# Performance work log

Measured on AMD Instinct MI355X. Metric: run time of the kernel, lower is better.

## Reference

```python
import jax, jax.numpy as jnp
import numpy as np

B, T, F, H = 256, 128, 256, 512

def _unif(key, shape, fan_in):
    stv = 1.0 / np.sqrt(fan_in)
    return jax.random.uniform(key, shape, jnp.float32, -stv, stv)

def setup_inputs() -> dict:
    key = jax.random.key(0)
    ks = jax.random.split(key, 20)
    x = jax.random.normal(ks[0], (B, T, F), jnp.float32)
    mask = (jax.random.uniform(ks[1], (B, T, F)) < 0.8).astype(jnp.float32)
    deltas = jax.random.uniform(ks[2], (B, T, F), jnp.float32) * 5.0
    return {
        'x': x, 'mask': mask, 'deltas': deltas,
        'W_gh': _unif(ks[3], (H, F), F), 'b_gh': jnp.zeros((H,), jnp.float32),
        'w_gx': _unif(ks[4], (F,), F), 'b_gx': jnp.zeros((F,), jnp.float32),
        'W_hist': _unif(ks[5], (F, H), H), 'b_hist': jnp.zeros((F,), jnp.float32),
        'W_fr': _unif(ks[6], (F, F), F), 'b_fr': jnp.zeros((F,), jnp.float32),
        'W_comb': _unif(ks[7], (F, 2 * F), 2 * F), 'b_comb': jnp.zeros((F,), jnp.float32),
        'W_ih': _unif(ks[8], (4 * H, 2 * F), 2 * F), 'b_ih': jnp.zeros((4 * H,), jnp.float32),
        'W_hh': _unif(ks[9], (4 * H, H), H), 'b_hh': jnp.zeros((4 * H,), jnp.float32),
    }

def reference(x, mask, deltas, W_gh, b_gh, w_gx, b_gx, W_hist, b_hist,
              W_fr, b_fr, W_comb, b_comb, W_ih, b_ih, W_hh, b_hh):
    dtype = x.dtype
    Fdim = x.shape[2]
    W_fr_m = W_fr * (1.0 - jnp.eye(Fdim, dtype=dtype))

    def step(carry, inp):
        h, c, loss = carry
        x_t, m_t, d_t = inp  # each [B, F]
        gamma_h = jnp.exp(-jax.nn.relu(d_t @ W_gh.T + b_gh))       # [B, H]
        h = h * gamma_h
        x_h = h @ W_hist.T + b_hist                                 # [B, F]
        x_r = m_t * x_t + (1.0 - m_t) * x_h
        xu = x_r @ W_fr_m.T + b_fr                                  # [B, F]
        gamma_x = jnp.exp(-jax.nn.relu(d_t * w_gx + b_gx))          # diag Decay
        beta = jax.nn.sigmoid(jnp.concatenate([gamma_x, m_t], axis=1) @ W_comb.T + b_comb)
        x_comb = beta * xu + (1.0 - beta) * x_h
        # MAE on observed entries, per step, accumulated
        loss = loss + jnp.sum(jnp.abs(x_comb - x_t) * m_t) / (jnp.sum(m_t) + 1e-12)
        x_imp = m_t * x_t + (1.0 - m_t) * x_comb
        rnn_in = jnp.concatenate([x_imp, m_t], axis=1)              # [B, 2F]
        gates = rnn_in @ W_ih.T + b_ih + h @ W_hh.T + b_hh          # [B, 4H]
        i_g, f_g, g_g, o_g = jnp.split(gates, 4, axis=1)
        i_g = jax.nn.sigmoid(i_g); f_g = jax.nn.sigmoid(f_g)
        g_g = jnp.tanh(g_g);       o_g = jax.nn.sigmoid(o_g)
        c = f_g * c + i_g * g_g
        h = o_g * jnp.tanh(c)
        return (h, c, loss), (x_imp, x_comb)

    Bdim, Hdim = x.shape[0], W_hh.shape[1]
    init = (jnp.zeros((Bdim, Hdim), dtype), jnp.zeros((Bdim, Hdim), dtype), jnp.zeros((), dtype))
    xs = (x.transpose(1, 0, 2), mask.transpose(1, 0, 2), deltas.transpose(1, 0, 2))
    (h, c, x_loss), (x_imp_seq, rec_seq) = jax.lax.scan(step, init, xs)
    x_imp = x_imp_seq.transpose(1, 0, 2)          # [B, T, F]
    reconstruction = rec_seq.transpose(1, 0, 2)   # [B, T, F]
    kl = jnp.zeros((), dtype)                     # non-bayesian
    return x_imp, reconstruction, h, x_loss, kl
```

## Files before the change

kernel.cpp:

```cpp
#include <hip/hip_runtime.h>
#include <hip/hip_bf16.h>

typedef float f32x4 __attribute__((ext_vector_type(4)));
typedef __bf16 bf16x8 __attribute__((ext_vector_type(8)));
typedef short s16x8 __attribute__((ext_vector_type(8)));
typedef unsigned short u16;
typedef unsigned long long u64;
typedef unsigned char u8;

constexpr int Bb = 256, Tt = 128, Ff = 256, Hh = 512;
constexpr int TF = Tt * Ff;
constexpr long OFF_RECON = (long)Bb * Tt * Ff;
constexpr long OFF_H     = 2L * Bb * Tt * Ff;
constexpr long OFF_LOSS  = OFF_H + (long)Bb * Hh;

__device__ inline float sigf(float v){ return 1.f / (1.f + expf(-v)); }
__device__ inline u16 f2b(float f){
  unsigned u = __float_as_uint(f);
  u += 0x7fffu + ((u >> 16) & 1u);
  return (u16)(u >> 16);
}
__device__ inline float b2f(u16 b){ return __uint_as_float(((unsigned)b) << 16); }

__device__ inline unsigned f2e4_sw(float f){
  unsigned u = __float_as_uint(f);
  unsigned s = (u >> 24) & 0x80u;
  int e = (int)((u >> 23) & 0xff) - 127;
  unsigned m = u & 0x7fffffu;
  if (((u >> 23) & 0xff) == 0xff) return s | 0x7e;
  if (e > 8 || (e == 8 && m > 0x600000)) return s | 0x7e;
  if (e < -10) return s;
  if (e >= -6) {
    unsigned keep = m >> 20, rest = m & 0xfffffu;
    keep += (rest > 0x80000u) || (rest == 0x80000u && (keep & 1));
    unsigned ee = (unsigned)(e + 7);
    if (keep == 8) { keep = 0; ee += 1; }
    if (ee >= 16) return s | 0x7e;
    return s | (ee << 3) | keep;
  }
  unsigned full = (1u << 23) | m;
  int shift = 20 + (-6 - e);
  unsigned keep = full >> shift;
  unsigned rest = full & ((1u << shift) - 1u);
  unsigned half = 1u << (shift - 1);
  keep += (rest > half) || (rest == half && (keep & 1));
  return s | keep;
}
__device__ inline unsigned f2e4(float f){
#if __has_builtin(__builtin_amdgcn_cvt_pk_fp8_f32)
  return (unsigned)__builtin_amdgcn_cvt_pk_fp8_f32(f, f, 0, false) & 0xffu;
#else
  return f2e4_sw(f);
#endif
}
__device__ inline unsigned pk2e4(float a, float b){
#if __has_builtin(__builtin_amdgcn_cvt_pk_fp8_f32)
  return (unsigned)__builtin_amdgcn_cvt_pk_fp8_f32(a, b, 0, false) & 0xffffu;
#else
  return f2e4_sw(a) | (f2e4_sw(b) << 8);
#endif
}

__device__ inline f32x4 mfma16(bf16x8 a, bf16x8 b, f32x4 c){
  return __builtin_amdgcn_mfma_f32_16x16x32_bf16(a, b, c, 0, 0, 0);
}
__device__ inline f32x4 mfma8(u64 a, u64 b, f32x4 c){
  return __builtin_amdgcn_mfma_f32_16x16x32_fp8_fp8((long)a, (long)b, c, 0, 0, 0);
}
__device__ inline bf16x8 ldb8(const u16* p){ return *reinterpret_cast<const bf16x8*>(p); }
__device__ inline bf16x8 cvt8(const float* p){
  const float4 a = ((const float4*)p)[0], b = ((const float4*)p)[1];
  s16x8 r;
  r[0]=f2b(a.x); r[1]=f2b(a.y); r[2]=f2b(a.z); r[3]=f2b(a.w);
  r[4]=f2b(b.x); r[5]=f2b(b.y); r[6]=f2b(b.z); r[7]=f2b(b.w);
  return __builtin_bit_cast(bf16x8, r);
}

enum { M_GH, M_BETA };

struct P {
  const float *x, *mask, *deltas;
  const float *b_gh, *w_gx, *b_gx, *b_comb;
  const u16 *Wgh, *Wcomb;
  u16 *gammah, *beta;
};

template<int MODE>
__global__ __launch_bounds__(256) void gk(P p)
{
  constexpr int K = (MODE==M_GH) ? 256 : 512;
  const int lane = threadIdx.x & 63;
  const int w = threadIdx.x >> 6;
  const int m0 = blockIdx.y*64 + (w>>1)*32;
  const int n0 = blockIdx.x*64 + (w&1)*32;
  const int fr = lane & 15;
  const int kg = (lane >> 4) << 3;

  f32x4 acc[2][2] = {};
  for (int k = 0; k < K; k += 32) {
    const int kk = k + kg;
    bf16x8 a[2], b[2];
    #pragma unroll
    for (int r = 0; r < 2; ++r) {
      const int mr = m0 + 16*r + fr;
      if constexpr (MODE == M_GH) {
        a[r] = cvt8(p.deltas + (size_t)mr*256 + kk);
      } else {
        if (kk < 256) {
          const float4 d0 = *(const float4*)(p.deltas + (size_t)mr*256 + kk);
          const float4 d1 = *(const float4*)(p.deltas + (size_t)mr*256 + kk + 4);
          const float4 w0 = *(const float4*)(p.w_gx + kk);
          const float4 w1 = *(const float4*)(p.w_gx + kk + 4);
          const float4 g0 = *(const float4*)(p.b_gx + kk);
          const float4 g1 = *(const float4*)(p.b_gx + kk + 4);
          s16x8 v;
          v[0]=f2b(expf(-fmaxf(d0.x*w0.x+g0.x,0.f)));
          v[1]=f2b(expf(-fmaxf(d0.y*w0.y+g0.y,0.f)));
          v[2]=f2b(expf(-fmaxf(d0.z*w0.z+g0.z,0.f)));
          v[3]=f2b(expf(-fmaxf(d0.w*w0.w+g0.w,0.f)));
          v[4]=f2b(expf(-fmaxf(d1.x*w1.x+g1.x,0.f)));
          v[5]=f2b(expf(-fmaxf(d1.y*w1.y+g1.y,0.f)));
          v[6]=f2b(expf(-fmaxf(d1.z*w1.z+g1.z,0.f)));
          v[7]=f2b(expf(-fmaxf(d1.w*w1.w+g1.w,0.f)));
          a[r] = __builtin_bit_cast(bf16x8, v);
        } else {
          a[r] = cvt8(p.mask + (size_t)mr*256 + (kk-256));
        }
      }
    }
    #pragma unroll
    for (int cc = 0; cc < 2; ++cc) {
      const int nr = n0 + 16*cc + fr;
      if constexpr (MODE == M_GH) b[cc] = ldb8(p.Wgh   + (size_t)nr*256 + kk);
      else                        b[cc] = ldb8(p.Wcomb + (size_t)nr*512 + kk);
    }
    #pragma unroll
    for (int r = 0; r < 2; ++r)
      #pragma unroll
      for (int cc = 0; cc < 2; ++cc)
        acc[r][cc] = mfma16(a[r], b[cc], acc[r][cc]);
  }

  #pragma unroll
  for (int r = 0; r < 2; ++r)
    #pragma unroll
    for (int cc = 0; cc < 2; ++cc)
      #pragma unroll
      for (int q = 0; q < 4; ++q) {
        const int m = m0 + 16*r + (lane>>4)*4 + q;
        const int n = n0 + 16*cc + (lane&15);
        const size_t tb = (size_t)(m & 127)*256 + (m >> 7);
        if constexpr (MODE == M_GH) {
          float v = expf(-fmaxf(acc[r][cc][q] + p.b_gh[n], 0.f));
          p.gammah[tb*512 + n] = f2b(v);
        } else {
          float v = sigf(acc[r][cc][q] + p.b_comb[n]);
          p.beta[tb*256 + n] = f2b(v);
        }
      }
}

constexpr int CV_TOT = 131072+131072+65536+131072;
__global__ __launch_bounds__(256) void k_conv(
    const float* Wgh, const float* Whist, const float* Wfr, const float* Wcomb,
    u16* ogh, u16* ohist, u16* ofr, u16* ocomb)
{
  int i = blockIdx.x*256 + threadIdx.x;
  if (i >= CV_TOT) return;
  int j = i;
  if (j < 131072) { ogh[j] = f2b(Wgh[j]); return; }       j -= 131072;
  if (j < 131072) { ohist[j] = f2b(Whist[j]); return; }   j -= 131072;
  if (j < 65536)  { ofr[j] = ((j>>8)==(j&255)) ? (u16)0 : f2b(Wfr[j]); return; } j -= 65536;
  ocomb[j] = f2b(Wcomb[j]);
}

__global__ __launch_bounds__(256) void k_conv8(
    const float* Wih, const float* Whh, u8* oih, u8* ohh)
{
  int i = blockIdx.x*256 + threadIdx.x;
  if (i < 524288) {
    ((u16*)oih)[i] = (u16)pk2e4(Wih[2*i], Wih[2*i+1]);
  } else {
    int j = i - 524288;
    ((u16*)ohh)[j] = (u16)pk2e4(Whh[2*j], Whh[2*j+1]);
  }
}

__global__ __launch_bounds__(256) void k_den(const float* __restrict__ mask,
                                             float* den, u8* mask8)
{
  const int t = blockIdx.x;
  const int f = threadIdx.x;
  float s = 0.f;
  for (int b = 0; b < Bb; ++b) {
    float mv = mask[(size_t)b*TF + (size_t)t*256 + f];
    s += mv;
    mask8[((size_t)t*256 + b)*256 + f] = (u8)f2e4(mv);
  }
  __shared__ float red[4];
  #pragma unroll
  for (int o = 32; o; o >>= 1) s += __shfl_down(s, o);
  if ((f & 63) == 0) red[f >> 6] = s;
  __syncthreads();
  if (f == 0) den[t] = red[0]+red[1]+red[2]+red[3];
}

__global__ void k_final(const float* num, const float* den, float* out)
{
  if (threadIdx.x < 64) {
    int t = threadIdx.x;
    float s = num[t]/(den[t]+1e-12f) + num[t+64]/(den[t+64]+1e-12f);
    #pragma unroll
    for (int o = 32; o; o >>= 1) s += __shfl_down(s, o);
    if (t == 0) { out[OFF_LOSS] = s; out[OFF_LOSS+1] = 0.f; }
  }
}

struct PSP {
  const float *x, *mask;
  const float *b_hist, *b_fr, *b_ih, *b_hh;
  const u16 *Whist, *Wfr, *gammah, *beta;
  const u8 *Wih8, *Whh8, *mask8;
  u16 *hb0, *hb1; u8 *h80, *h81;
  float *num, *out;
  unsigned *flags; int *xcc;
};

__global__ __launch_bounds__(512, 1) void k_loopP(PSP p)
{
  __shared__ char smem[22016];
  float* pre_s  = (float*)smem;
  u16*   xr_s   = (u16*)smem;
  u8*    ximp_s = (u8*)(smem + 17408);
  __shared__ int s_fast;

  const int tid = threadIdx.x, lane = tid & 63, w = tid >> 6;
  const int fr = lane & 15, kg = (lane >> 4) << 3;
  const int bid = blockIdx.x;
  const int slab = bid & 15, cg = bid >> 4;
  const int m0 = slab*16, hc0 = cg*64;

  if (tid == 0) {
    unsigned xv;
    asm volatile("s_getreg_b32 %0, hwreg(HW_REG_XCC_ID)" : "=s"(xv));
    __hip_atomic_store(p.xcc + bid, (int)(xv & 15u) + 1, __ATOMIC_RELAXED, __HIP_MEMORY_SCOPE_AGENT);
    int v0 = 0, ok = 1;
    #pragma unroll 1
    for (int j = 0; j < 8; ++j) {
      int v; unsigned spin = 0;
      do {
        v = __hip_atomic_load(p.xcc + slab + 16*j, __ATOMIC_RELAXED, __HIP_MEMORY_SCOPE_AGENT);
        if (v) break;
        __builtin_amdgcn_s_sleep(8);
      } while (++spin < (1u<<22));
      if (j == 0) v0 = v;
      ok &= (v != 0) && (v == v0);
    }
    s_fast = ok;
  }
  __syncthreads();
  const int fast = s_fast;

  const int nA0 = w * 32;
  float bh[2], bf2[2];
  #pragma unroll
  for (int cc = 0; cc < 2; ++cc) {
    bh[cc]  = p.b_hist[nA0 + cc*16 + fr];
    bf2[cc] = p.b_fr  [nA0 + cc*16 + fr];
  }
  const int gB = w >> 1, half = w & 1;
  const int lrow = tid >> 5, lcolp = (tid & 31) * 2;
  float bsum[4][2];
  #pragma unroll
  for (int g = 0; g < 4; ++g)
    #pragma unroll
    for (int j = 0; j < 2; ++j) {
      const int n = hc0 + lcolp + j;
      bsum[g][j] = p.b_ih[g*512 + n] + p.b_hh[g*512 + n];
    }
  float c0 = 0.f, c1 = 0.f;

  for (int t = 0; t < Tt; ++t) {
    const u16* hr  = (t & 1) ? p.hb1 : p.hb0;
    u16*       hw  = (t & 1) ? p.hb0 : p.hb1;
    const u8*  h8r = (t & 1) ? p.h81 : p.h80;
    u8*        h8w = (t & 1) ? p.h80 : p.h81;

    if (t > 0) {
      if (w == 0 && lane < 8) {
        const unsigned tgt = (unsigned)t;
        unsigned* mf = p.flags + (size_t)(slab + 16*lane)*16;
        unsigned spin = 0;
        if (fast) {
          while (__hip_atomic_load(mf, __ATOMIC_RELAXED, __HIP_MEMORY_SCOPE_AGENT) < tgt
                 && spin < (1u<<24)) { __builtin_amdgcn_s_sleep(1); ++spin; }
        } else {
          while (__hip_atomic_load(mf, __ATOMIC_ACQUIRE, __HIP_MEMORY_SCOPE_AGENT) < tgt
                 && spin < (1u<<24)) { __builtin_amdgcn_s_sleep(1); ++spin; }
        }
      }
      __syncthreads();
      __builtin_amdgcn_sched_barrier(0);
    }

    bf16x8 ah[16];
    {
      const u16* hb = hr + (size_t)(m0 + fr)*512 + kg;
      #pragma unroll
      for (int i = 0; i < 16; ++i) {
        const u16* pa = hb + i*32;
        asm volatile("global_load_dwordx4 %0, %1, off sc0" : "=&v"(ah[i]) : "v"(pa));
      }
      asm volatile("s_waitcnt vmcnt(0)" ::: "memory");
      __builtin_amdgcn_sched_barrier(0);
    }
    f32x4 acc[2] = {};
    #pragma unroll
    for (int k = 0; k < 16; ++k) {
      #pragma unroll
      for (int cc = 0; cc < 2; ++cc)
        acc[cc] = mfma16(ah[k], ldb8(p.Whist + (size_t)(nA0 + cc*16 + fr)*512 + k*32 + kg), acc[cc]);
    }
    float xhv[8];
    #pragma unroll
    for (int cc = 0; cc < 2; ++cc)
      #pragma unroll
      for (int q = 0; q < 4; ++q) {
        const int row = (lane>>4)*4 + q;
        const int n   = nA0 + cc*16 + fr;
        const float v = acc[cc][q] + bh[cc];
        xhv[cc*4+q] = v;
        const size_t gi = (size_t)(m0+row)*TF + (size_t)t*256 + n;
        const float mm = p.mask[gi];
        const float xx = p.x[gi];
        xr_s[row*264 + n] = f2b(mm*xx + (1.f-mm)*v);
      }
    __syncthreads();

    f32x4 acc2[2] = {};
    #pragma unroll
    for (int k = 0; k < 8; ++k) {
      bf16x8 a = *(const bf16x8*)(xr_s + fr*264 + k*32 + kg);
      #pragma unroll
      for (int cc = 0; cc < 2; ++cc)
        acc2[cc] = mfma16(a, ldb8(p.Wfr + (size_t)(nA0 + cc*16 + fr)*256 + k*32 + kg), acc2[cc]);
    }
    float lnum = 0.f;
    #pragma unroll
    for (int cc = 0; cc < 2; ++cc)
      #pragma unroll
      for (int q = 0; q < 4; ++q) {
        const int row = (lane>>4)*4 + q;
        const int n   = nA0 + cc*16 + fr;
        const float xu  = acc2[cc][q] + bf2[cc];
        const float bet = b2f(p.beta[((size_t)t*256 + m0+row)*256 + n]);
        const float xc  = bet*xu + (1.f-bet)*xhv[cc*4+q];
        const size_t gi = (size_t)(m0+row)*TF + (size_t)t*256 + n;
        const float mm = p.mask[gi];
        const float xx = p.x[gi];
        const float xi = mm*xx + (1.f-mm)*xc;
        ximp_s[row*272 + n] = (u8)f2e4(xi);
        if (cg == 0) {
          __builtin_nontemporal_store(xc, p.out + OFF_RECON + gi);
          __builtin_nontemporal_store(xi, p.out + gi);
          lnum += fabsf(xc - xx)*mm;
        }
      }
    if (cg == 0) {
      #pragma unroll
      for (int o = 32; o; o >>= 1) lnum += __shfl_down(lnum, o);
      if (lane == 0) atomicAdd(p.num + t, lnum);
    }
    __syncthreads();

    u64 a8[16];
    {
      const u8* h8b = h8r + (size_t)(m0 + fr)*512 + kg;
      #pragma unroll
      for (int i = 0; i < 16; ++i) {
        const u8* pa = h8b + i*32;
        asm volatile("global_load_dwordx2 %0, %1, off sc0" : "=&v"(a8[i]) : "v"(pa));
      }
    }
    f32x4 ag[2] = {};
    #pragma unroll
    for (int k = 0; k < 8; ++k) {
      const u64 a = *(const u64*)(ximp_s + (size_t)fr*272 + k*32 + kg);
      #pragma unroll
      for (int cc = 0; cc < 2; ++cc)
        ag[cc] = mfma8(a, *(const u64*)(p.Wih8 + (size_t)(gB*512 + hc0 + half*32 + cc*16 + fr)*512 + k*32 + kg), ag[cc]);
    }
    #pragma unroll
    for (int k = 0; k < 8; ++k) {
      const u64 a = *(const u64*)(p.mask8 + ((size_t)t*256 + m0 + fr)*256 + k*32 + kg);
      #pragma unroll
      for (int cc = 0; cc < 2; ++cc)
        ag[cc] = mfma8(a, *(const u64*)(p.Wih8 + (size_t)(gB*512 + hc0 + half*32 + cc*16 + fr)*512 + 256 + k*32 + kg), ag[cc]);
    }
    asm volatile("s_waitcnt vmcnt(0)" ::: "memory");
    __builtin_amdgcn_sched_barrier(0);
    #pragma unroll
    for (int k = 0; k < 16; ++k) {
      #pragma unroll
      for (int cc = 0; cc < 2; ++cc)
        ag[cc] = mfma8(a8[k], *(const u64*)(p.Whh8 + (size_t)(gB*512 + hc0 + half*32 + cc*16 + fr)*512 + k*32 + kg), ag[cc]);
    }
    #pragma unroll
    for (int cc = 0; cc < 2; ++cc)
      #pragma unroll
      for (int q = 0; q < 4; ++q) {
        const int row = (lane>>4)*4 + q;
        const int col = half*32 + cc*16 + fr;
        pre_s[(gB*16 + row)*68 + col] = ag[cc][q];
      }
    __syncthreads();

    {
      float hvv[2];
      {
        const float pi = pre_s[(0*16 + lrow)*68 + lcolp] + bsum[0][0];
        const float pf = pre_s[(1*16 + lrow)*68 + lcolp] + bsum[1][0];
        const float pg = pre_s[(2*16 + lrow)*68 + lcolp] + bsum[2][0];
        const float po = pre_s[(3*16 + lrow)*68 + lcolp] + bsum[3][0];
        const float cv = sigf(pf)*c0 + sigf(pi)*tanhf(pg);
        c0 = cv; hvv[0] = sigf(po)*tanhf(cv);
      }
      {
        const float pi = pre_s[(0*16 + lrow)*68 + lcolp+1] + bsum[0][1];
        const float pf = pre_s[(1*16 + lrow)*68 + lcolp+1] + bsum[1][1];
        const float pg = pre_s[(2*16 + lrow)*68 + lcolp+1] + bsum[2][1];
        const float po = pre_s[(3*16 + lrow)*68 + lcolp+1] + bsum[3][1];
        const float cv = sigf(pf)*c1 + sigf(pi)*tanhf(pg);
        c1 = cv; hvv[1] = sigf(po)*tanhf(cv);
      }
      const int idx0 = (m0+lrow)*512 + hc0 + lcolp;
      if (t == Tt-1) {
        __builtin_nontemporal_store(hvv[0], p.out + OFF_H + idx0);
        __builtin_nontemporal_store(hvv[1], p.out + OFF_H + idx0 + 1);
      } else {
        float hd[2];
        #pragma unroll
        for (int j = 0; j < 2; ++j) {
          const float gn = b2f(__builtin_nontemporal_load(
              p.gammah + ((size_t)(t+1)*256 + m0 + lrow)*512 + hc0 + lcolp + j));
          hd[j] = hvv[j]*gn;
        }
        union { unsigned u; u16 h[2]; } pb2;
        pb2.h[0] = f2b(hd[0]); pb2.h[1] = f2b(hd[1]);
        *(unsigned*)(hw + idx0) = pb2.u;
        *(u16*)(h8w + idx0) = (u16)pk2e4(hd[0], hd[1]);
      }
    }

    if (t < Tt-1) {
      asm volatile("s_waitcnt vmcnt(0)" ::: "memory");
      __syncthreads();
      if (tid == 0) {
        if (fast)
          __hip_atomic_store(p.flags + (size_t)bid*16, (unsigned)(t+1),
                             __ATOMIC_RELAXED, __HIP_MEMORY_SCOPE_AGENT);
        else
          __hip_atomic_store(p.flags + (size_t)bid*16, (unsigned)(t+1),
                             __ATOMIC_RELEASE, __HIP_MEMORY_SCOPE_AGENT);
      }
    }
  }
}

extern "C" void kernel_launch(void* const* d_in, const int* in_sizes, int n_in,
                              void* d_out, int out_size, void* d_ws, size_t ws_size,
                              hipStream_t stream)
{
  char* wsb = (char*)d_ws;
  unsigned* flags = (unsigned*)(wsb + 0);
  int*      xcc   = (int*)(wsb + 8192);
  float*    num   = (float*)(wsb + 8704);
  u16*  hb0    = (u16*)(wsb + 9216);
  u8*   h80    = (u8*)(wsb + 271360);
  u16*  hb1    = (u16*)(wsb + 402432);
  u8*   h81    = (u8*)(wsb + 664576);
  float* den   = (float*)(wsb + 795648);
  u8*   mask8  = (u8*)(wsb + 796160);
  u16*  beta   = (u16*)(wsb + 9184768);
  u16*  gammah = (u16*)(wsb + 25961984);
  u16*  Whist  = (u16*)(wsb + 59516416);
  u16*  Wfr    = (u16*)(wsb + 59778560);
  u16*  Wgh    = (u16*)(wsb + 59909632);
  u16*  Wcomb  = (u16*)(wsb + 60171776);
  u8*   Wih8   = (u8*)(wsb + 60433920);
  u8*   Whh8   = (u8*)(wsb + 61482496);

  hipMemsetAsync(d_ws, 0, 402432, stream);

  k_conv<<<dim3((CV_TOT+255)/256), dim3(256), 0, stream>>>(
      (const float*)d_in[3], (const float*)d_in[7], (const float*)d_in[9],
      (const float*)d_in[11], Wgh, Whist, Wfr, Wcomb);
  k_conv8<<<dim3(4096), dim3(256), 0, stream>>>(
      (const float*)d_in[13], (const float*)d_in[15], Wih8, Whh8);
  k_den<<<dim3(128), dim3(256), 0, stream>>>((const float*)d_in[1], den, mask8);

  P p{};
  p.x = (const float*)d_in[0];  p.mask = (const float*)d_in[1];
  p.deltas = (const float*)d_in[2];
  p.b_gh = (const float*)d_in[4];  p.w_gx = (const float*)d_in[5];
  p.b_gx = (const float*)d_in[6];  p.b_comb = (const float*)d_in[12];
  p.Wgh = Wgh; p.Wcomb = Wcomb;
  p.gammah = gammah; p.beta = beta;
  gk<M_GH><<<dim3(8, 512), dim3(256), 0, stream>>>(p);
  gk<M_BETA><<<dim3(4, 512), dim3(256), 0, stream>>>(p);

  PSP ps{};
  ps.x = (const float*)d_in[0];  ps.mask = (const float*)d_in[1];
  ps.b_hist = (const float*)d_in[8];  ps.b_fr = (const float*)d_in[10];
  ps.b_ih = (const float*)d_in[14];   ps.b_hh = (const float*)d_in[16];
  ps.Whist = Whist; ps.Wfr = Wfr; ps.gammah = gammah; ps.beta = beta;
  ps.Wih8 = Wih8; ps.Whh8 = Whh8; ps.mask8 = mask8;
  ps.hb0 = hb0; ps.hb1 = hb1; ps.h80 = h80; ps.h81 = h81;
  ps.num = num; ps.out = (float*)d_out;
  ps.flags = flags; ps.xcc = xcc;
  k_loopP<<<dim3(128), dim3(512), 0, stream>>>(ps);

  k_final<<<dim3(1), dim3(64), 0, stream>>>(num, den, (float*)d_out);
}
```

Measured before the change: 5.047 ms.

## Prefetch per-step inputs before the barrier and defer output stores past flag release

Loads x, mask, beta and the next-step gamma_h at the start of each timestep, before the inter-block spin wait, so their latency overlaps the wait. The fp8 h loads are issued earlier, alongside the W_hist MFMA phase. The recon and x_imp global stores move to after the flag release so they stay off the critical path of the recurrence. The spin sleep length is also raised, and the loss accumulation now runs unconditionally, which adds some register pressure.

```diff
diff --git a/kernel.cpp b/kernel.cpp
--- a/kernel.cpp
+++ b/kernel.cpp
@@ -286,6 +286,23 @@
     const u8*  h8r = (t & 1) ? p.h81 : p.h80;
     u8*        h8w = (t & 1) ? p.h80 : p.h81;
 
+    float mmv[8], xxv[8]; u16 betv[8];
+    #pragma unroll
+    for (int cc = 0; cc < 2; ++cc)
+      #pragma unroll
+      for (int q = 0; q < 4; ++q) {
+        const int e = cc*4 + q;
+        const int row = (lane>>4)*4 + q;
+        const int n   = nA0 + cc*16 + fr;
+        const size_t gi = (size_t)(m0+row)*TF + (size_t)t*256 + n;
+        xxv[e] = p.x[gi];
+        mmv[e] = p.mask[gi];
+        betv[e] = p.beta[((size_t)t*256 + m0+row)*256 + n];
+      }
+    unsigned gnw = 0;
+    if (t < Tt-1)
+      gnw = *(const unsigned*)(p.gammah + ((size_t)(t+1)*256 + m0 + lrow)*512 + hc0 + lcolp);
+
     if (t > 0) {
       if (w == 0 && lane < 8) {
         const unsigned tgt = (unsigned)t;
@@ -293,10 +310,10 @@
         unsigned spin = 0;
         if (fast) {
           while (__hip_atomic_load(mf, __ATOMIC_RELAXED, __HIP_MEMORY_SCOPE_AGENT) < tgt
-                 && spin < (1u<<24)) { __builtin_amdgcn_s_sleep(1); ++spin; }
+                 && spin < (1u<<24)) { __builtin_amdgcn_s_sleep(8); ++spin; }
         } else {
           while (__hip_atomic_load(mf, __ATOMIC_ACQUIRE, __HIP_MEMORY_SCOPE_AGENT) < tgt
-                 && spin < (1u<<24)) { __builtin_amdgcn_s_sleep(1); ++spin; }
+                 && spin < (1u<<24)) { __builtin_amdgcn_s_sleep(8); ++spin; }
         }
       }
       __syncthreads();
@@ -314,6 +331,16 @@
       asm volatile("s_waitcnt vmcnt(0)" ::: "memory");
       __builtin_amdgcn_sched_barrier(0);
     }
+    u64 a8[16];
+    {
+      const u8* h8b = h8r + (size_t)(m0 + fr)*512 + kg;
+      #pragma unroll
+      for (int i = 0; i < 16; ++i) {
+        const u8* pa = h8b + i*32;
+        asm volatile("global_load_dwordx2 %0, %1, off sc0" : "=&v"(a8[i]) : "v"(pa));
+      }
+    }
+
     f32x4 acc[2] = {};
     #pragma unroll
     for (int k = 0; k < 16; ++k) {
@@ -326,14 +353,12 @@
     for (int cc = 0; cc < 2; ++cc)
       #pragma unroll
       for (int q = 0; q < 4; ++q) {
+        const int e = cc*4 + q;
         const int row = (lane>>4)*4 + q;
         const int n   = nA0 + cc*16 + fr;
         const float v = acc[cc][q] + bh[cc];
-        xhv[cc*4+q] = v;
-        const size_t gi = (size_t)(m0+row)*TF + (size_t)t*256 + n;
-        const float mm = p.mask[gi];
-        const float xx = p.x[gi];
-        xr_s[row*264 + n] = f2b(mm*xx + (1.f-mm)*v);
+        xhv[e] = v;
+        xr_s[row*264 + n] = f2b(mmv[e]*xxv[e] + (1.f-mmv[e])*v);
       }
     __syncthreads();
 
@@ -345,26 +370,21 @@
       for (int cc = 0; cc < 2; ++cc)
         acc2[cc] = mfma16(a, ldb8(p.Wfr + (size_t)(nA0 + cc*16 + fr)*256 + k*32 + kg), acc2[cc]);
     }
-    float lnum = 0.f;
+    float xcv[8], xiv[8], lnum = 0.f;
     #pragma unroll
     for (int cc = 0; cc < 2; ++cc)
       #pragma unroll
       for (int q = 0; q < 4; ++q) {
+        const int e = cc*4 + q;
         const int row = (lane>>4)*4 + q;
         const int n   = nA0 + cc*16 + fr;
         const float xu  = acc2[cc][q] + bf2[cc];
-        const float bet = b2f(p.beta[((size_t)t*256 + m0+row)*256 + n]);
-        const float xc  = bet*xu + (1.f-bet)*xhv[cc*4+q];
-        const size_t gi = (size_t)(m0+row)*TF + (size_t)t*256 + n;
-        const float mm = p.mask[gi];
-        const float xx = p.x[gi];
-        const float xi = mm*xx + (1.f-mm)*xc;
+        const float bet = b2f(betv[e]);
+        const float xc  = bet*xu + (1.f-bet)*xhv[e];
+        const float xi  = mmv[e]*xxv[e] + (1.f-mmv[e])*xc;
         ximp_s[row*272 + n] = (u8)f2e4(xi);
-        if (cg == 0) {
-          __builtin_nontemporal_store(xc, p.out + OFF_RECON + gi);
-          __builtin_nontemporal_store(xi, p.out + gi);
-          lnum += fabsf(xc - xx)*mm;
-        }
+        xcv[e] = xc; xiv[e] = xi;
+        lnum += fabsf(xc - xxv[e])*mmv[e];
       }
     if (cg == 0) {
       #pragma unroll
@@ -373,15 +393,6 @@
     }
     __syncthreads();
 
-    u64 a8[16];
-    {
-      const u8* h8b = h8r + (size_t)(m0 + fr)*512 + kg;
-      #pragma unroll
-      for (int i = 0; i < 16; ++i) {
-        const u8* pa = h8b + i*32;
-        asm volatile("global_load_dwordx2 %0, %1, off sc0" : "=&v"(a8[i]) : "v"(pa));
-      }
-    }
     f32x4 ag[2] = {};
     #pragma unroll
     for (int k = 0; k < 8; ++k) {
@@ -438,17 +449,13 @@
         __builtin_nontemporal_store(hvv[0], p.out + OFF_H + idx0);
         __builtin_nontemporal_store(hvv[1], p.out + OFF_H + idx0 + 1);
       } else {
-        float hd[2];
-        #pragma unroll
-        for (int j = 0; j < 2; ++j) {
-          const float gn = b2f(__builtin_nontemporal_load(
-              p.gammah + ((size_t)(t+1)*256 + m0 + lrow)*512 + hc0 + lcolp + j));
-          hd[j] = hvv[j]*gn;
-        }
+        const float gn0 = b2f((u16)(gnw & 0xffffu));
+        const float gn1 = b2f((u16)(gnw >> 16));
+        const float hd0 = hvv[0]*gn0, hd1 = hvv[1]*gn1;
         union { unsigned u; u16 h[2]; } pb2;
-        pb2.h[0] = f2b(hd[0]); pb2.h[1] = f2b(hd[1]);
+        pb2.h[0] = f2b(hd0); pb2.h[1] = f2b(hd1);
         *(unsigned*)(hw + idx0) = pb2.u;
-        *(u16*)(h8w + idx0) = (u16)pk2e4(hd[0], hd[1]);
+        *(u16*)(h8w + idx0) = (u16)pk2e4(hd0, hd1);
       }
     }
 
@@ -463,6 +470,20 @@
           __hip_atomic_store(p.flags + (size_t)bid*16, (unsigned)(t+1),
                              __ATOMIC_RELEASE, __HIP_MEMORY_SCOPE_AGENT);
       }
+    }
+
+    if (cg == 0) {
+      #pragma unroll
+      for (int cc = 0; cc < 2; ++cc)
+        #pragma unroll
+        for (int q = 0; q < 4; ++q) {
+          const int e = cc*4 + q;
+          const int row = (lane>>4)*4 + q;
+          const int n   = nA0 + cc*16 + fr;
+          const size_t gi = (size_t)(m0+row)*TF + (size_t)t*256 + n;
+          __builtin_nontemporal_store(xcv[e], p.out + OFF_RECON + gi);
+          __builtin_nontemporal_store(xiv[e], p.out + gi);
+        }
     }
   }
 }
```

New measurement: 4.915 ms. -2.6%, faster.

## Use 1024-thread persistent blocks with W_hh cached in LDS and prefetched step inputs

Applied to the files above, without the earlier changes.

The persistent LSTM kernel goes from 512 to 1024 threads per block, so each wave now handles a single 16-column tile instead of two. At kernel start each block copies its W_hh fp8 slice (128 KB) into XOR-swizzled LDS, so the recurrent GEMM no longer reads weights from global or L2 on every step. The h tile is staged once through LDS instead of being loaded per wave, and x, mask, beta and gammah are fetched before the inter-block flag wait. Output stores are moved after the flag release, and the spin-wait sleep is made longer. The change relies on about 160 KB of dynamic LDS per block, and the larger block raises register pressure and synchronisation cost.

```diff
diff --git a/kernel.cpp b/kernel.cpp
--- a/kernel.cpp
+++ b/kernel.cpp
@@ -226,12 +226,14 @@
   unsigned *flags; int *xcc;
 };
 
-__global__ __launch_bounds__(512, 1) void k_loopP(PSP p)
-{
-  __shared__ char smem[22016];
-  float* pre_s  = (float*)smem;
-  u16*   xr_s   = (u16*)smem;
-  u8*    ximp_s = (u8*)(smem + 17408);
+__global__ __launch_bounds__(1024, 4) void k_loopP(PSP p)
+{
+  extern __shared__ char smem[];
+  u8*    whh_s  = (u8*)smem;
+  u16*   h_s    = (u16*)(smem + 131072);
+  float* pre_s  = (float*)(smem + 131072);
+  u16*   xr_s   = (u16*)(smem + 147968);
+  u8*    ximp_s = (u8*)(smem + 156416);
   __shared__ int s_fast;
 
   const int tid = threadIdx.x, lane = tid & 63, w = tid >> 6;
@@ -258,33 +260,46 @@
     }
     s_fast = ok;
   }
+
+  for (int i = tid; i < 8192; i += 1024) {
+    const int row = i >> 5;
+    const int kk  = (i & 31) << 4;
+    const int g = row >> 6, c = row & 63;
+    const float4 v = *(const float4*)(p.Whh8 + ((size_t)(g*512 + hc0 + c) << 9) + kk);
+    *(float4*)(whh_s + ((size_t)row << 9) + (kk ^ ((row & 7) << 4))) = v;
+  }
   __syncthreads();
   const int fast = s_fast;
 
-  const int nA0 = w * 32;
-  float bh[2], bf2[2];
-  #pragma unroll
-  for (int cc = 0; cc < 2; ++cc) {
-    bh[cc]  = p.b_hist[nA0 + cc*16 + fr];
-    bf2[cc] = p.b_fr  [nA0 + cc*16 + fr];
-  }
-  const int gB = w >> 1, half = w & 1;
-  const int lrow = tid >> 5, lcolp = (tid & 31) * 2;
-  float bsum[4][2];
+  const int nA0 = w * 16;
+  const float bh  = p.b_hist[nA0 + fr];
+  const float bfv = p.b_fr  [nA0 + fr];
+  const int gB = w & 3, qh = w >> 2;
+  float bsum[4];
   #pragma unroll
   for (int g = 0; g < 4; ++g)
-    #pragma unroll
-    for (int j = 0; j < 2; ++j) {
-      const int n = hc0 + lcolp + j;
-      bsum[g][j] = p.b_ih[g*512 + n] + p.b_hh[g*512 + n];
-    }
-  float c0 = 0.f, c1 = 0.f;
+    bsum[g] = p.b_ih[g*512 + hc0 + lane] + p.b_hh[g*512 + hc0 + lane];
+  float c0 = 0.f;
 
   for (int t = 0; t < Tt; ++t) {
     const u16* hr  = (t & 1) ? p.hb1 : p.hb0;
     u16*       hw  = (t & 1) ? p.hb0 : p.hb1;
     const u8*  h8r = (t & 1) ? p.h81 : p.h80;
     u8*        h8w = (t & 1) ? p.h80 : p.h81;
+
+    float mmv[4], xxv[4]; u16 betv[4];
+    #pragma unroll
+    for (int q = 0; q < 4; ++q) {
+      const int row = (lane>>4)*4 + q;
+      const int n   = nA0 + fr;
+      const size_t gi = (size_t)(m0+row)*TF + (size_t)t*256 + n;
+      xxv[q] = p.x[gi];
+      mmv[q] = p.mask[gi];
+      betv[q] = p.beta[((size_t)t*256 + m0+row)*256 + n];
+    }
+    u16 gnv = 0;
+    if (t < Tt-1)
+      gnv = p.gammah[((size_t)(t+1)*256 + m0 + w)*512 + hc0 + lane];
 
     if (t > 0) {
       if (w == 0 && lane < 8) {
@@ -293,79 +308,63 @@
         unsigned spin = 0;
         if (fast) {
           while (__hip_atomic_load(mf, __ATOMIC_RELAXED, __HIP_MEMORY_SCOPE_AGENT) < tgt
-                 && spin < (1u<<24)) { __builtin_amdgcn_s_sleep(1); ++spin; }
+                 && spin < (1u<<24)) { __builtin_amdgcn_s_sleep(8); ++spin; }
         } else {
           while (__hip_atomic_load(mf, __ATOMIC_ACQUIRE, __HIP_MEMORY_SCOPE_AGENT) < tgt
-                 && spin < (1u<<24)) { __builtin_amdgcn_s_sleep(1); ++spin; }
+                 && spin < (1u<<24)) { __builtin_amdgcn_s_sleep(8); ++spin; }
         }
       }
       __syncthreads();
       __builtin_amdgcn_sched_barrier(0);
     }
 
-    bf16x8 ah[16];
     {
-      const u16* hb = hr + (size_t)(m0 + fr)*512 + kg;
-      #pragma unroll
-      for (int i = 0; i < 16; ++i) {
-        const u16* pa = hb + i*32;
-        asm volatile("global_load_dwordx4 %0, %1, off sc0" : "=&v"(ah[i]) : "v"(pa));
-      }
-      asm volatile("s_waitcnt vmcnt(0)" ::: "memory");
-      __builtin_amdgcn_sched_barrier(0);
-    }
-    f32x4 acc[2] = {};
+      bf16x8 hv;
+      const u16* src = hr + (size_t)(m0 + w)*512 + lane*8;
+      asm volatile("global_load_dwordx4 %0, %1, off sc0\n\ts_waitcnt vmcnt(0)"
+                   : "=v"(hv) : "v"(src) : "memory");
+      *(bf16x8*)(h_s + w*520 + lane*8) = hv;
+    }
+    __syncthreads();
+
+    f32x4 acc = {};
     #pragma unroll
     for (int k = 0; k < 16; ++k) {
-      #pragma unroll
-      for (int cc = 0; cc < 2; ++cc)
-        acc[cc] = mfma16(ah[k], ldb8(p.Whist + (size_t)(nA0 + cc*16 + fr)*512 + k*32 + kg), acc[cc]);
-    }
-    float xhv[8];
-    #pragma unroll
-    for (int cc = 0; cc < 2; ++cc)
-      #pragma unroll
-      for (int q = 0; q < 4; ++q) {
-        const int row = (lane>>4)*4 + q;
-        const int n   = nA0 + cc*16 + fr;
-        const float v = acc[cc][q] + bh[cc];
-        xhv[cc*4+q] = v;
-        const size_t gi = (size_t)(m0+row)*TF + (size_t)t*256 + n;
-        const float mm = p.mask[gi];
-        const float xx = p.x[gi];
-        xr_s[row*264 + n] = f2b(mm*xx + (1.f-mm)*v);
-      }
+      bf16x8 a = *(const bf16x8*)(h_s + fr*520 + k*32 + kg);
+      bf16x8 b = ldb8(p.Whist + (size_t)(nA0 + fr)*512 + k*32 + kg);
+      acc = mfma16(a, b, acc);
+    }
+    float xhv[4];
+    #pragma unroll
+    for (int q = 0; q < 4; ++q) {
+      const int row = (lane>>4)*4 + q;
+      const int n   = nA0 + fr;
+      const float v = acc[q] + bh;
+      xhv[q] = v;
+      xr_s[row*264 + n] = f2b(mmv[q]*xxv[q] + (1.f-mmv[q])*v);
+    }
     __syncthreads();
 
-    f32x4 acc2[2] = {};
+    f32x4 acc2 = {};
     #pragma unroll
     for (int k = 0; k < 8; ++k) {
       bf16x8 a = *(const bf16x8*)(xr_s + fr*264 + k*32 + kg);
-      #pragma unroll
-      for (int cc = 0; cc < 2; ++cc)
-        acc2[cc] = mfma16(a, ldb8(p.Wfr + (size_t)(nA0 + cc*16 + fr)*256 + k*32 + kg), acc2[cc]);
-    }
-    float lnum = 0.f;
-    #pragma unroll
-    for (int cc = 0; cc < 2; ++cc)
-      #pragma unroll
-      for (int q = 0; q < 4; ++q) {
-        const int row = (lane>>4)*4 + q;
-        const int n   = nA0 + cc*16 + fr;
-        const float xu  = acc2[cc][q] + bf2[cc];
-        const float bet = b2f(p.beta[((size_t)t*256 + m0+row)*256 + n]);
-        const float xc  = bet*xu + (1.f-bet)*xhv[cc*4+q];
-        const size_t gi = (size_t)(m0+row)*TF + (size_t)t*256 + n;
-        const float mm = p.mask[gi];
-        const float xx = p.x[gi];
-        const float xi = mm*xx + (1.f-mm)*xc;
-        ximp_s[row*272 + n] = (u8)f2e4(xi);
-        if (cg == 0) {
-          __builtin_nontemporal_store(xc, p.out + OFF_RECON + gi);
-          __builtin_nontemporal_store(xi, p.out + gi);
-          lnum += fabsf(xc - xx)*mm;
-        }
-      }
+      bf16x8 b = ldb8(p.Wfr + (size_t)(nA0 + fr)*256 + k*32 + kg);
+      acc2 = mfma16(a, b, acc2);
+    }
+    float xcv[4], xiv[4], lnum = 0.f;
+    #pragma unroll
+    for (int q = 0; q < 4; ++q) {
+      const int row = (lane>>4)*4 + q;
+      const int n   = nA0 + fr;
+      const float xu  = acc2[q] + bfv;
+      const float bet = b2f(betv[q]);
+      const float xc  = bet*xu + (1.f-bet)*xhv[q];
+      const float xi  = mmv[q]*xxv[q] + (1.f-mmv[q])*xc;
+      ximp_s[row*264 + n] = (u8)f2e4(xi);
+      xcv[q] = xc; xiv[q] = xi;
+      lnum += fabsf(xc - xxv[q])*mmv[q];
+    }
     if (cg == 0) {
       #pragma unroll
       for (int o = 32; o; o >>= 1) lnum += __shfl_down(lnum, o);
@@ -382,73 +381,52 @@
         asm volatile("global_load_dwordx2 %0, %1, off sc0" : "=&v"(a8[i]) : "v"(pa));
       }
     }
-    f32x4 ag[2] = {};
+    f32x4 ag = {};
     #pragma unroll
     for (int k = 0; k < 8; ++k) {
-      const u64 a = *(const u64*)(ximp_s + (size_t)fr*272 + k*32 + kg);
-      #pragma unroll
-      for (int cc = 0; cc < 2; ++cc)
-        ag[cc] = mfma8(a, *(const u64*)(p.Wih8 + (size_t)(gB*512 + hc0 + half*32 + cc*16 + fr)*512 + k*32 + kg), ag[cc]);
+      const u64 a = *(const u64*)(ximp_s + (size_t)fr*264 + k*32 + kg);
+      const u64 b = *(const u64*)(p.Wih8 + (size_t)(gB*512 + hc0 + qh*16 + fr)*512 + k*32 + kg);
+      ag = mfma8(a, b, ag);
     }
     #pragma unroll
     for (int k = 0; k < 8; ++k) {
       const u64 a = *(const u64*)(p.mask8 + ((size_t)t*256 + m0 + fr)*256 + k*32 + kg);
-      #pragma unroll
-      for (int cc = 0; cc < 2; ++cc)
-        ag[cc] = mfma8(a, *(const u64*)(p.Wih8 + (size_t)(gB*512 + hc0 + half*32 + cc*16 + fr)*512 + 256 + k*32 + kg), ag[cc]);
+      const u64 b = *(const u64*)(p.Wih8 + (size_t)(gB*512 + hc0 + qh*16 + fr)*512 + 256 + k*32 + kg);
+      ag = mfma8(a, b, ag);
     }
     asm volatile("s_waitcnt vmcnt(0)" ::: "memory");
     __builtin_amdgcn_sched_barrier(0);
-    #pragma unroll
-    for (int k = 0; k < 16; ++k) {
+    {
+      const int wrow = gB*64 + qh*16 + fr;
+      const int wsw  = (wrow & 7) << 4;
       #pragma unroll
-      for (int cc = 0; cc < 2; ++cc)
-        ag[cc] = mfma8(a8[k], *(const u64*)(p.Whh8 + (size_t)(gB*512 + hc0 + half*32 + cc*16 + fr)*512 + k*32 + kg), ag[cc]);
-    }
-    #pragma unroll
-    for (int cc = 0; cc < 2; ++cc)
-      #pragma unroll
-      for (int q = 0; q < 4; ++q) {
-        const int row = (lane>>4)*4 + q;
-        const int col = half*32 + cc*16 + fr;
-        pre_s[(gB*16 + row)*68 + col] = ag[cc][q];
-      }
+      for (int k = 0; k < 16; ++k) {
+        const u64 b = *(const u64*)(whh_s + ((size_t)wrow << 9) + ((k*32 + kg) ^ wsw));
+        ag = mfma8(a8[k], b, ag);
+      }
+    }
+    #pragma unroll
+    for (int q = 0; q < 4; ++q) {
+      const int row = (lane>>4)*4 + q;
+      pre_s[(gB*16 + row)*66 + qh*16 + fr] = ag[q];
+    }
     __syncthreads();
 
     {
-      float hvv[2];
-      {
-        const float pi = pre_s[(0*16 + lrow)*68 + lcolp] + bsum[0][0];
-        const float pf = pre_s[(1*16 + lrow)*68 + lcolp] + bsum[1][0];
-        const float pg = pre_s[(2*16 + lrow)*68 + lcolp] + bsum[2][0];
-        const float po = pre_s[(3*16 + lrow)*68 + lcolp] + bsum[3][0];
-        const float cv = sigf(pf)*c0 + sigf(pi)*tanhf(pg);
-        c0 = cv; hvv[0] = sigf(po)*tanhf(cv);
-      }
-      {
-        const float pi = pre_s[(0*16 + lrow)*68 + lcolp+1] + bsum[0][1];
-        const float pf = pre_s[(1*16 + lrow)*68 + lcolp+1] + bsum[1][1];
-        const float pg = pre_s[(2*16 + lrow)*68 + lcolp+1] + bsum[2][1];
-        const float po = pre_s[(3*16 + lrow)*68 + lcolp+1] + bsum[3][1];
-        const float cv = sigf(pf)*c1 + sigf(pi)*tanhf(pg);
-        c1 = cv; hvv[1] = sigf(po)*tanhf(cv);
-      }
-      const int idx0 = (m0+lrow)*512 + hc0 + lcolp;
+      const float pi = pre_s[(0*16 + w)*66 + lane] + bsum[0];
+      const float pf = pre_s[(1*16 + w)*66 + lane] + bsum[1];
+      const float pg = pre_s[(2*16 + w)*66 + lane] + bsum[2];
+      const float po = pre_s[(3*16 + w)*66 + lane] + bsum[3];
+      const float cv = sigf(pf)*c0 + sigf(pi)*tanhf(pg);
+      c0 = cv;
+      const float hv = sigf(po)*tanhf(cv);
+      const int idx = (m0+w)*512 + hc0 + lane;
       if (t == Tt-1) {
-        __builtin_nontemporal_store(hvv[0], p.out + OFF_H + idx0);
-        __builtin_nontemporal_store(hvv[1], p.out + OFF_H + idx0 + 1);
+        __builtin_nontemporal_store(hv, p.out + OFF_H + idx);
       } else {
-        float hd[2];
-        #pragma unroll
-        for (int j = 0; j < 2; ++j) {
-          const float gn = b2f(__builtin_nontemporal_load(
-              p.gammah + ((size_t)(t+1)*256 + m0 + lrow)*512 + hc0 + lcolp + j));
-          hd[j] = hvv[j]*gn;
-        }
-        union { unsigned u; u16 h[2]; } pb2;
-        pb2.h[0] = f2b(hd[0]); pb2.h[1] = f2b(hd[1]);
-        *(unsigned*)(hw + idx0) = pb2.u;
-        *(u16*)(h8w + idx0) = (u16)pk2e4(hd[0], hd[1]);
+        const float hd = hv * b2f(gnv);
+        hw[idx]  = f2b(hd);
+        h8w[idx] = (u8)f2e4(hd);
       }
     }
 
@@ -462,6 +440,17 @@
         else
           __hip_atomic_store(p.flags + (size_t)bid*16, (unsigned)(t+1),
                              __ATOMIC_RELEASE, __HIP_MEMORY_SCOPE_AGENT);
+      }
+    }
+
+    if (cg == 0) {
+      #pragma unroll
+      for (int q = 0; q < 4; ++q) {
+        const int row = (lane>>4)*4 + q;
+        const int n   = nA0 + fr;
+        const size_t gi = (size_t)(m0+row)*TF + (size_t)t*256 + n;
+        __builtin_nontemporal_store(xcv[q], p.out + OFF_RECON + gi);
+        __builtin_nontemporal_store(xiv[q], p.out + gi);
       }
     }
   }
@@ -518,7 +507,10 @@
   ps.hb0 = hb0; ps.hb1 = hb1; ps.h80 = h80; ps.h81 = h81;
   ps.num = num; ps.out = (float*)d_out;
   ps.flags = flags; ps.xcc = xcc;
-  k_loopP<<<dim3(128), dim3(512), 0, stream>>>(ps);
+
+  (void)hipFuncSetAttribute((const void*)k_loopP,
+      hipFuncAttributeMaxDynamicSharedMemorySize, 160640);
+  k_loopP<<<dim3(128), dim3(1024), 160640, stream>>>(ps);
 
   k_final<<<dim3(1), dim3(64), 0, stream>>>(num, den, (float*)d_out);
 }
```

Result: faster. 4.886 ms (-3.2%).
